# Kernel optimization log

Measured on AMD Instinct MI355X. Metric: run time of the kernel, lower is better.

The kernel has to match this reference:

```python
import jax, jax.numpy as jnp
import numpy as np
import math

TWO_PI = 2.0 * math.pi
B, K, DIM = 8, 1024, 4096
TEMP = 10.0  # softmax temperature from `sims * 10`


def setup_inputs() -> dict:
    key = jax.random.key(0)
    k1, k2 = jax.random.split(key)
    superposed = jax.random.uniform(k1, (B, DIM), jnp.float32, 0.0, TWO_PI)
    codebook = jax.random.uniform(k2, (K, DIM), jnp.float32, 0.0, TWO_PI)
    return {"superposed": superposed, "codebook": codebook, "num_iterations": 50}


def _cos_sim(est, codebook):
    # est: (B, dim), codebook: (K, dim) -> (B, K) mean cosine of phase diff
    return jnp.cos(est[:, None, :] - codebook[None, :, :]).mean(axis=-1)


def reference(superposed, codebook, num_iterations):
    # Batched resonator decode: iteratively refine estimate toward codebook
    # entries via softmax-weighted phasor superposition (torch.angle == atan2).
    cb_cos = jnp.cos(codebook)  # (K, dim) real part of codebook phasors
    cb_sin = jnp.sin(codebook)  # (K, dim) imag part

    def step(est, _):
        sims = _cos_sim(est, codebook)                 # (B, K)
        w = jax.nn.softmax(sims * TEMP, axis=-1)       # (B, K)
        re = w @ cb_cos                                # (B, dim)
        im = w @ cb_sin                                # (B, dim)
        est_new = jnp.arctan2(im, re) % TWO_PI         # angle of complex sum
        return est_new, None

    est, _ = jax.lax.scan(step, superposed, None, length=num_iterations)
    return _cos_sim(est, codebook)  # (B, K) final similarity scores
```

## Files before the change

### kernel.cpp

```cpp
#include <hip/hip_runtime.h>
#include <hip/hip_fp16.h>
#include <math.h>


#define KCODES 1024
#define DIMS   4096
#define BATCH  8
#define NITER_MAX 50
#define NSLICE 256

#define T1_SZF   (DIMS * 2 * KCODES / 2)
#define EST_OFF  (T1_SZF)
#define EST_SZ   (DIMS * 2 * BATCH)
#define W_OFF    (EST_OFF + EST_SZ)
#define W_SZ     (BATCH * KCODES)
#define P_OFF    (W_OFF + W_SZ)

#define C2 (0.00244140625f * 1.4426950408889634f)

__device__ __forceinline__ ushort f2bf(float x) {
  unsigned u = __float_as_uint(x);
  return (ushort)((u + 0x7FFFu + ((u >> 16) & 1u)) >> 16);
}
__device__ __forceinline__ float bf2f(ushort u) {
  return __uint_as_float(((unsigned)u) << 16);
}

template <int CTRL>
__device__ __forceinline__ float dpp_add(float x) {
  int v = __builtin_amdgcn_update_dpp(0, __float_as_int(x), CTRL, 0xF, 0xF, false);
  return x + __int_as_float(v);
}
__device__ __forceinline__ float wave_sum64(float x) {
  x = dpp_add<0x111>(x);
  x = dpp_add<0x112>(x);
  x = dpp_add<0x114>(x);
  x = dpp_add<0x118>(x);
  x = dpp_add<0x142>(x);
  x = dpp_add<0x143>(x);
  return x;
}

__global__ __launch_bounds__(256) void k_trig(const float* __restrict__ cb,
                                              float* __restrict__ ws) {
  __shared__ float lc[64][65], ls[64][65];
  const int t  = threadIdx.x;
  const int bk = blockIdx.x & 15;
  const int bd = blockIdx.x >> 4;
  const int k0 = bk * 64, d0 = bd * 64;
  const int c = t & 63;
  #pragma unroll
  for (int i = 0; i < 16; ++i) {
    const int r = (t >> 6) + i * 4;
    float a = cb[(size_t)(k0 + r) * DIMS + d0 + c];
    float s, cc; sincosf(a, &s, &cc);
    lc[r][c] = cc; ls[r][c] = s;
  }
  __syncthreads();
  ushort* T1 = (ushort*)ws;
  #pragma unroll
  for (int j = 0; j < 16; ++j) {
    const int dd = (t >> 6) + j * 4;
    T1[(size_t)((d0 + dd) * 2 + 0) * KCODES + k0 + c] = f2bf(lc[c][dd]);
    T1[(size_t)((d0 + dd) * 2 + 1) * KCODES + k0 + c] = f2bf(ls[c][dd]);
  }
}

__global__ __launch_bounds__(256) void k_init(const float* __restrict__ sup,
                                              float* __restrict__ ws) {
  float* EST = ws + EST_OFF;
  const int i = blockIdx.x * 256 + threadIdx.x;
  const int b = i >> 12, d = i & 4095;
  float s, c; sincosf(sup[(size_t)b * DIMS + d], &s, &c);
  EST[(d * 2 + 0) * BATCH + b] = c;
  EST[(d * 2 + 1) * BATCH + b] = s;
}

__global__ __launch_bounds__(256) void k_sims0(float* __restrict__ ws) {
  const ushort* T1  = (const ushort*)ws;
  const float*  EST = ws + EST_OFF;
  __half* P = (__half*)(ws + P_OFF);
  const int t  = threadIdx.x;
  const int ds = blockIdx.x;
  const int r0 = ds * 32;
  const int k4 = t * 4;

  float4 acc[BATCH];
  #pragma unroll
  for (int b = 0; b < BATCH; ++b) acc[b] = make_float4(0.f, 0.f, 0.f, 0.f);

  #pragma unroll 8
  for (int r = 0; r < 32; ++r) {
    const int row = r0 + r;
    const ushort4 tu = *(const ushort4*)&T1[(size_t)row * KCODES + k4];
    const float4 tv = make_float4(bf2f(tu.x), bf2f(tu.y), bf2f(tu.z), bf2f(tu.w));
    const float4 e0 = *(const float4*)&EST[row * BATCH + 0];
    const float4 e1 = *(const float4*)&EST[row * BATCH + 4];
    const float ev[8] = {e0.x, e0.y, e0.z, e0.w, e1.x, e1.y, e1.z, e1.w};
    #pragma unroll
    for (int b = 0; b < BATCH; ++b) {
      acc[b].x = fmaf(ev[b], tv.x, acc[b].x);
      acc[b].y = fmaf(ev[b], tv.y, acc[b].y);
      acc[b].z = fmaf(ev[b], tv.z, acc[b].z);
      acc[b].w = fmaf(ev[b], tv.w, acc[b].w);
    }
  }
  #pragma unroll
  for (int b = 0; b < BATCH; ++b) {
    __half* pp = &P[(size_t)ds * (BATCH * KCODES) + b * KCODES + k4];
    *(__half2*)(pp + 0) = __floats2half2_rn(acc[b].x, acc[b].y);
    *(__half2*)(pp + 2) = __floats2half2_rn(acc[b].z, acc[b].w);
  }
}

__global__ __launch_bounds__(256) void k_wexp(float* __restrict__ ws,
                                              const int* __restrict__ nit_p,
                                              int it) {
  if (it >= *nit_p) return;
  const __half* P = (const __half*)(ws + P_OFF);
  float* W = ws + W_OFF;
  __shared__ float scr[128];
  const int t = threadIdx.x, lane = t & 63, wv = t >> 6;
  const int b2 = blockIdx.x >> 5;
  const int k0 = (blockIdx.x & 31) * 32;

  float4 raw[4];
  const float4* p4 =
      (const float4*)(P + (size_t)t * (BATCH * KCODES) + b2 * KCODES + k0);
  raw[0] = p4[0]; raw[1] = p4[1]; raw[2] = p4[2]; raw[3] = p4[3];
  const __half2* h2 = (const __half2*)raw;
  #pragma unroll
  for (int kk = 0; kk < 16; ++kk) {
    const float2 f2 = __half22float2(h2[kk]);
    const float s0 = wave_sum64(f2.x);
    const float s1 = wave_sum64(f2.y);
    if (lane == 63) {
      scr[wv * 32 + 2 * kk + 0] = s0;
      scr[wv * 32 + 2 * kk + 1] = s1;
    }
  }
  __syncthreads();
  if (t < 32) {
    const float s = scr[t] + scr[32 + t] + scr[64 + t] + scr[96 + t];
    W[b2 * KCODES + k0 + t] = exp2f(s * C2);
  }
}

__global__ __launch_bounds__(512) void k_fused(float* __restrict__ ws,
                                               const int* __restrict__ nit_p,
                                               int it) {
  if (it >= *nit_p) return;
  const ushort* T1 = (const ushort*)ws;
  const float*  Wg = ws + W_OFF;
  __half* P = (__half*)(ws + P_OFF);

  __shared__ float smem[BATCH * KCODES];
  __shared__ float est_l[32 * BATCH];

  const int t = threadIdx.x, lane = t & 63, wv = t >> 6;
  const int r0 = blockIdx.x * 32;

  #pragma unroll
  for (int j = 0; j < 4; ++j) {
    const int idx = (j * 512 + t) * 4;
    *(float4*)&smem[idx] = *(const float4*)&Wg[idx];
  }
  __syncthreads();

  const int rw = wv * 4;
  float acc[4][BATCH];
  #pragma unroll
  for (int r = 0; r < 4; ++r)
    #pragma unroll
    for (int b = 0; b < BATCH; ++b) acc[r][b] = 0.f;

  #pragma unroll
  for (int c = 0; c < 4; ++c) {
    const int kk = c * 256 + lane * 4;
    float4 wr[BATCH];
    #pragma unroll
    for (int b = 0; b < BATCH; ++b)
      wr[b] = *(const float4*)&smem[b * KCODES + kk];
    #pragma unroll
    for (int r = 0; r < 4; ++r) {
      const ushort4 tu = *(const ushort4*)&T1[(size_t)(r0 + rw + r) * KCODES + kk];
      const float4 tv = make_float4(bf2f(tu.x), bf2f(tu.y), bf2f(tu.z), bf2f(tu.w));
      #pragma unroll
      for (int b = 0; b < BATCH; ++b) {
        acc[r][b] = fmaf(wr[b].x, tv.x, acc[r][b]);
        acc[r][b] = fmaf(wr[b].y, tv.y, acc[r][b]);
        acc[r][b] = fmaf(wr[b].z, tv.z, acc[r][b]);
        acc[r][b] = fmaf(wr[b].w, tv.w, acc[r][b]);
      }
    }
  }
  #pragma unroll
  for (int r = 0; r < 4; ++r)
    #pragma unroll
    for (int b = 0; b < BATCH; ++b) {
      const float s = wave_sum64(acc[r][b]);
      if (lane == 63) est_l[(rw + r) * BATCH + b] = s;
    }
  __syncthreads();

  if (t < 128) {
    const int dl = t >> 3, b = t & 7;
    const float re = est_l[(2 * dl + 0) * BATCH + b];
    const float im = est_l[(2 * dl + 1) * BATCH + b];
    const float n2 = fmaf(re, re, im * im);
    float ec, es;
    if (n2 > 0.f) {
      const float inv = rsqrtf(n2);
      ec = re * inv; es = im * inv;
    } else { ec = 1.f; es = 0.f; }
    est_l[(2 * dl + 0) * BATCH + b] = ec;
    est_l[(2 * dl + 1) * BATCH + b] = es;
  }
  __syncthreads();

  const int half = t >> 8, tk = t & 255, k4 = tk * 4;
  const int rb = half * 16;
  float4 a[BATCH];
  #pragma unroll
  for (int b = 0; b < BATCH; ++b) a[b] = make_float4(0.f, 0.f, 0.f, 0.f);

  #pragma unroll
  for (int r = 0; r < 16; ++r) {
    const int lr = rb + r;
    const ushort4 tu = *(const ushort4*)&T1[(size_t)(r0 + lr) * KCODES + k4];
    const float4 tv = make_float4(bf2f(tu.x), bf2f(tu.y), bf2f(tu.z), bf2f(tu.w));
    const float4 e0 = *(const float4*)&est_l[lr * BATCH + 0];
    const float4 e1 = *(const float4*)&est_l[lr * BATCH + 4];
    const float ev[8] = {e0.x, e0.y, e0.z, e0.w, e1.x, e1.y, e1.z, e1.w};
    #pragma unroll
    for (int b = 0; b < BATCH; ++b) {
      a[b].x = fmaf(ev[b], tv.x, a[b].x);
      a[b].y = fmaf(ev[b], tv.y, a[b].y);
      a[b].z = fmaf(ev[b], tv.z, a[b].z);
      a[b].w = fmaf(ev[b], tv.w, a[b].w);
    }
  }
  if (half == 1) {
    #pragma unroll
    for (int b = 0; b < BATCH; ++b)
      *(float4*)&smem[(b * 256 + tk) * 4] = a[b];
  }
  __syncthreads();
  if (half == 0) {
    #pragma unroll
    for (int b = 0; b < BATCH; ++b) {
      const float4 o = *(const float4*)&smem[(b * 256 + tk) * 4];
      __half* pp = &P[(size_t)blockIdx.x * (BATCH * KCODES) + b * KCODES + k4];
      *(__half2*)(pp + 0) = __floats2half2_rn(a[b].x + o.x, a[b].y + o.y);
      *(__half2*)(pp + 2) = __floats2half2_rn(a[b].z + o.z, a[b].w + o.w);
    }
  }
}

__global__ __launch_bounds__(256) void k_out(const float* __restrict__ ws,
                                             float* __restrict__ out) {
  const __half* P = (const __half*)(ws + P_OFF);
  __shared__ float scr[128];
  const int t = threadIdx.x, lane = t & 63, wv = t >> 6;
  const int b2 = blockIdx.x >> 5;
  const int k0 = (blockIdx.x & 31) * 32;

  float4 raw[4];
  const float4* p4 =
      (const float4*)(P + (size_t)t * (BATCH * KCODES) + b2 * KCODES + k0);
  raw[0] = p4[0]; raw[1] = p4[1]; raw[2] = p4[2]; raw[3] = p4[3];
  const __half2* h2 = (const __half2*)raw;
  #pragma unroll
  for (int kk = 0; kk < 16; ++kk) {
    const float2 f2 = __half22float2(h2[kk]);
    const float s0 = wave_sum64(f2.x);
    const float s1 = wave_sum64(f2.y);
    if (lane == 63) {
      scr[wv * 32 + 2 * kk + 0] = s0;
      scr[wv * 32 + 2 * kk + 1] = s1;
    }
  }
  __syncthreads();
  if (t < 32) {
    const float s = scr[t] + scr[32 + t] + scr[64 + t] + scr[96 + t];
    out[b2 * KCODES + k0 + t] = s * (1.0f / (float)DIMS);
  }
}

extern "C" void kernel_launch(void* const* d_in, const int* in_sizes, int n_in,
                              void* d_out, int out_size, void* d_ws, size_t ws_size,
                              hipStream_t stream) {
  const float* sup = (const float*)d_in[0];
  const float* cbk = (const float*)d_in[1];
  const int*   nit = (const int*)d_in[2];
  float* outp = (float*)d_out;
  float* ws   = (float*)d_ws;

  hipLaunchKernelGGL(k_trig,  dim3(1024), dim3(256), 0, stream, cbk, ws);
  hipLaunchKernelGGL(k_init,  dim3(128),  dim3(256), 0, stream, sup, ws);
  hipLaunchKernelGGL(k_sims0, dim3(256),  dim3(256), 0, stream, ws);

  for (int it = 0; it < NITER_MAX; ++it) {
    hipLaunchKernelGGL(k_wexp,  dim3(256), dim3(256), 0, stream, ws, nit, it);
    hipLaunchKernelGGL(k_fused, dim3(256), dim3(512), 0, stream, ws, nit, it);
  }
  hipLaunchKernelGGL(k_out, dim3(256), dim3(256), 0, stream, ws, outp);
}
```

Measured before the change: 729.3 us.

## Compute sims per codeword block from transposed table instead of split-K partials

Adds a second bf16 codebook table laid out codeword-major, so each block computes full similarity dot products for four codewords over all dims. The half-precision partial-sum buffer and the separate reduction kernel are removed. The estimate-update kernel now only normalizes and writes the new estimate, and the sim/exp kernel also produces the final output. This drops the partial-sum round trip through global memory and the fp16 rounding of partials. In exchange it doubles table storage, and every block reads the whole estimate vector.

```diff
diff --git a/kernel.cpp b/kernel.cpp
--- a/kernel.cpp
+++ b/kernel.cpp
@@ -1,20 +1,19 @@
 #include <hip/hip_runtime.h>
-#include <hip/hip_fp16.h>
 #include <math.h>
 
 
 #define KCODES 1024
 #define DIMS   4096
 #define BATCH  8
+#define JROWS  (DIMS * 2)
 #define NITER_MAX 50
-#define NSLICE 256
-
-#define T1_SZF   (DIMS * 2 * KCODES / 2)
-#define EST_OFF  (T1_SZF)
-#define EST_SZ   (DIMS * 2 * BATCH)
-#define W_OFF    (EST_OFF + EST_SZ)
-#define W_SZ     (BATCH * KCODES)
-#define P_OFF    (W_OFF + W_SZ)
+
+#define T1_SZF  (JROWS * KCODES / 2)
+#define T2_OFF  (T1_SZF)
+#define T2_SZF  (T1_SZF)
+#define EST_OFF (T2_OFF + T2_SZF)
+#define EST_SZ  (JROWS * BATCH)
+#define W_OFF   (EST_OFF + EST_SZ)
 
 #define C2 (0.00244140625f * 1.4426950408889634f)
 
@@ -66,95 +65,110 @@
   }
 }
 
+__global__ __launch_bounds__(256) void k_trig2(const float* __restrict__ cb,
+                                               float* __restrict__ ws) {
+  __shared__ float cbl[4][DIMS];
+  const int t = threadIdx.x;
+  const int g = blockIdx.x;
+  #pragma unroll
+  for (int c = 0; c < 4; ++c)
+    #pragma unroll
+    for (int q = 0; q < 4; ++q) {
+      const int off = (q * 256 + t) * 4;
+      *(float4*)&cbl[c][off] = *(const float4*)&cb[(size_t)(4 * g + c) * DIMS + off];
+    }
+  __syncthreads();
+
+  ushort buf[128];
+  #pragma unroll
+  for (int dl = 0; dl < 16; ++dl) {
+    #pragma unroll
+    for (int c = 0; c < 4; ++c) {
+      float s, cc; sincosf(cbl[c][16 * t + dl], &s, &cc);
+      buf[(2 * dl + 0) * 4 + c] = f2bf(cc);
+      buf[(2 * dl + 1) * 4 + c] = f2bf(s);
+    }
+  }
+  uint4* dst = (uint4*)((ushort*)(ws + T2_OFF) + (size_t)g * (JROWS * 4) + t * 128);
+  const uint4* src = (const uint4*)buf;
+  #pragma unroll
+  for (int i = 0; i < 16; ++i) dst[i] = src[i];
+}
+
 __global__ __launch_bounds__(256) void k_init(const float* __restrict__ sup,
                                               float* __restrict__ ws) {
   float* EST = ws + EST_OFF;
   const int i = blockIdx.x * 256 + threadIdx.x;
   const int b = i >> 12, d = i & 4095;
   float s, c; sincosf(sup[(size_t)b * DIMS + d], &s, &c);
-  EST[(d * 2 + 0) * BATCH + b] = c;
-  EST[(d * 2 + 1) * BATCH + b] = s;
-}
-
-__global__ __launch_bounds__(256) void k_sims0(float* __restrict__ ws) {
-  const ushort* T1  = (const ushort*)ws;
+  EST[(2 * d + 0) * BATCH + b] = c;
+  EST[(2 * d + 1) * BATCH + b] = s;
+}
+
+__global__ __launch_bounds__(512) void k_simw(float* __restrict__ ws,
+                                              const int* __restrict__ nit_p,
+                                              float* __restrict__ out,
+                                              int it) {
+  const int NI = *nit_p;
+  if (it > NI) return;
+  const ushort* T2  = (const ushort*)(ws + T2_OFF);
   const float*  EST = ws + EST_OFF;
-  __half* P = (__half*)(ws + P_OFF);
-  const int t  = threadIdx.x;
-  const int ds = blockIdx.x;
-  const int r0 = ds * 32;
-  const int k4 = t * 4;
-
-  float4 acc[BATCH];
-  #pragma unroll
-  for (int b = 0; b < BATCH; ++b) acc[b] = make_float4(0.f, 0.f, 0.f, 0.f);
-
-  #pragma unroll 8
-  for (int r = 0; r < 32; ++r) {
-    const int row = r0 + r;
-    const ushort4 tu = *(const ushort4*)&T1[(size_t)row * KCODES + k4];
-    const float4 tv = make_float4(bf2f(tu.x), bf2f(tu.y), bf2f(tu.z), bf2f(tu.w));
-    const float4 e0 = *(const float4*)&EST[row * BATCH + 0];
-    const float4 e1 = *(const float4*)&EST[row * BATCH + 4];
+  float* W = ws + W_OFF;
+  __shared__ float scr[8 * 32];
+
+  const int t = threadIdx.x, lane = t & 63, wv = t >> 6;
+  const int g = blockIdx.x;
+  const ushort* trow = T2 + (size_t)g * (JROWS * 4);
+
+  float acc[4][BATCH];
+  #pragma unroll
+  for (int c = 0; c < 4; ++c)
+    #pragma unroll
+    for (int b = 0; b < BATCH; ++b) acc[c][b] = 0.f;
+
+  #pragma unroll 4
+  for (int i = 0; i < 16; ++i) {
+    const int j = i * 512 + t;
+    const float4 e0 = *(const float4*)&EST[j * BATCH + 0];
+    const float4 e1 = *(const float4*)&EST[j * BATCH + 4];
     const float ev[8] = {e0.x, e0.y, e0.z, e0.w, e1.x, e1.y, e1.z, e1.w};
+    const ushort4 tu = *(const ushort4*)&trow[j * 4];
+    const float tc[4] = {bf2f(tu.x), bf2f(tu.y), bf2f(tu.z), bf2f(tu.w)};
+    #pragma unroll
+    for (int c = 0; c < 4; ++c)
+      #pragma unroll
+      for (int b = 0; b < BATCH; ++b)
+        acc[c][b] = fmaf(tc[c], ev[b], acc[c][b]);
+  }
+
+  #pragma unroll
+  for (int c = 0; c < 4; ++c)
     #pragma unroll
     for (int b = 0; b < BATCH; ++b) {
-      acc[b].x = fmaf(ev[b], tv.x, acc[b].x);
-      acc[b].y = fmaf(ev[b], tv.y, acc[b].y);
-      acc[b].z = fmaf(ev[b], tv.z, acc[b].z);
-      acc[b].w = fmaf(ev[b], tv.w, acc[b].w);
-    }
-  }
-  #pragma unroll
-  for (int b = 0; b < BATCH; ++b) {
-    __half* pp = &P[(size_t)ds * (BATCH * KCODES) + b * KCODES + k4];
-    *(__half2*)(pp + 0) = __floats2half2_rn(acc[b].x, acc[b].y);
-    *(__half2*)(pp + 2) = __floats2half2_rn(acc[b].z, acc[b].w);
-  }
-}
-
-__global__ __launch_bounds__(256) void k_wexp(float* __restrict__ ws,
-                                              const int* __restrict__ nit_p,
-                                              int it) {
-  if (it >= *nit_p) return;
-  const __half* P = (const __half*)(ws + P_OFF);
-  float* W = ws + W_OFF;
-  __shared__ float scr[128];
-  const int t = threadIdx.x, lane = t & 63, wv = t >> 6;
-  const int b2 = blockIdx.x >> 5;
-  const int k0 = (blockIdx.x & 31) * 32;
-
-  float4 raw[4];
-  const float4* p4 =
-      (const float4*)(P + (size_t)t * (BATCH * KCODES) + b2 * KCODES + k0);
-  raw[0] = p4[0]; raw[1] = p4[1]; raw[2] = p4[2]; raw[3] = p4[3];
-  const __half2* h2 = (const __half2*)raw;
-  #pragma unroll
-  for (int kk = 0; kk < 16; ++kk) {
-    const float2 f2 = __half22float2(h2[kk]);
-    const float s0 = wave_sum64(f2.x);
-    const float s1 = wave_sum64(f2.y);
-    if (lane == 63) {
-      scr[wv * 32 + 2 * kk + 0] = s0;
-      scr[wv * 32 + 2 * kk + 1] = s1;
-    }
-  }
-  __syncthreads();
+      const float s = wave_sum64(acc[c][b]);
+      if (lane == 63) scr[wv * 32 + c * BATCH + b] = s;
+    }
+  __syncthreads();
+
   if (t < 32) {
-    const float s = scr[t] + scr[32 + t] + scr[64 + t] + scr[96 + t];
-    W[b2 * KCODES + k0 + t] = exp2f(s * C2);
-  }
-}
-
-__global__ __launch_bounds__(512) void k_fused(float* __restrict__ ws,
-                                               const int* __restrict__ nit_p,
-                                               int it) {
+    float s = 0.f;
+    #pragma unroll
+    for (int w8 = 0; w8 < 8; ++w8) s += scr[w8 * 32 + t];
+    const int c = t >> 3, b = t & 7;
+    if (it == NI) out[b * KCODES + 4 * g + c] = s * (1.0f / (float)DIMS);
+    else          W[b * KCODES + 4 * g + c] = exp2f(s * C2);
+  }
+}
+
+__global__ __launch_bounds__(512) void k_est(float* __restrict__ ws,
+                                             const int* __restrict__ nit_p,
+                                             int it) {
   if (it >= *nit_p) return;
   const ushort* T1 = (const ushort*)ws;
   const float*  Wg = ws + W_OFF;
-  __half* P = (__half*)(ws + P_OFF);
-
-  __shared__ float smem[BATCH * KCODES];
+  float* EST = ws + EST_OFF;
+
+  __shared__ float Wl[BATCH * KCODES];
   __shared__ float est_l[32 * BATCH];
 
   const int t = threadIdx.x, lane = t & 63, wv = t >> 6;
@@ -163,7 +177,7 @@
   #pragma unroll
   for (int j = 0; j < 4; ++j) {
     const int idx = (j * 512 + t) * 4;
-    *(float4*)&smem[idx] = *(const float4*)&Wg[idx];
+    *(float4*)&Wl[idx] = *(const float4*)&Wg[idx];
   }
   __syncthreads();
 
@@ -180,7 +194,7 @@
     float4 wr[BATCH];
     #pragma unroll
     for (int b = 0; b < BATCH; ++b)
-      wr[b] = *(const float4*)&smem[b * KCODES + kk];
+      wr[b] = *(const float4*)&Wl[b * KCODES + kk];
     #pragma unroll
     for (int r = 0; r < 4; ++r) {
       const ushort4 tu = *(const ushort4*)&T1[(size_t)(r0 + rw + r) * KCODES + kk];
@@ -218,73 +232,7 @@
   }
   __syncthreads();
 
-  const int half = t >> 8, tk = t & 255, k4 = tk * 4;
-  const int rb = half * 16;
-  float4 a[BATCH];
-  #pragma unroll
-  for (int b = 0; b < BATCH; ++b) a[b] = make_float4(0.f, 0.f, 0.f, 0.f);
-
-  #pragma unroll
-  for (int r = 0; r < 16; ++r) {
-    const int lr = rb + r;
-    const ushort4 tu = *(const ushort4*)&T1[(size_t)(r0 + lr) * KCODES + k4];
-    const float4 tv = make_float4(bf2f(tu.x), bf2f(tu.y), bf2f(tu.z), bf2f(tu.w));
-    const float4 e0 = *(const float4*)&est_l[lr * BATCH + 0];
-    const float4 e1 = *(const float4*)&est_l[lr * BATCH + 4];
-    const float ev[8] = {e0.x, e0.y, e0.z, e0.w, e1.x, e1.y, e1.z, e1.w};
-    #pragma unroll
-    for (int b = 0; b < BATCH; ++b) {
-      a[b].x = fmaf(ev[b], tv.x, a[b].x);
-      a[b].y = fmaf(ev[b], tv.y, a[b].y);
-      a[b].z = fmaf(ev[b], tv.z, a[b].z);
-      a[b].w = fmaf(ev[b], tv.w, a[b].w);
-    }
-  }
-  if (half == 1) {
-    #pragma unroll
-    for (int b = 0; b < BATCH; ++b)
-      *(float4*)&smem[(b * 256 + tk) * 4] = a[b];
-  }
-  __syncthreads();
-  if (half == 0) {
-    #pragma unroll
-    for (int b = 0; b < BATCH; ++b) {
-      const float4 o = *(const float4*)&smem[(b * 256 + tk) * 4];
-      __half* pp = &P[(size_t)blockIdx.x * (BATCH * KCODES) + b * KCODES + k4];
-      *(__half2*)(pp + 0) = __floats2half2_rn(a[b].x + o.x, a[b].y + o.y);
-      *(__half2*)(pp + 2) = __floats2half2_rn(a[b].z + o.z, a[b].w + o.w);
-    }
-  }
-}
-
-__global__ __launch_bounds__(256) void k_out(const float* __restrict__ ws,
-                                             float* __restrict__ out) {
-  const __half* P = (const __half*)(ws + P_OFF);
-  __shared__ float scr[128];
-  const int t = threadIdx.x, lane = t & 63, wv = t >> 6;
-  const int b2 = blockIdx.x >> 5;
-  const int k0 = (blockIdx.x & 31) * 32;
-
-  float4 raw[4];
-  const float4* p4 =
-      (const float4*)(P + (size_t)t * (BATCH * KCODES) + b2 * KCODES + k0);
-  raw[0] = p4[0]; raw[1] = p4[1]; raw[2] = p4[2]; raw[3] = p4[3];
-  const __half2* h2 = (const __half2*)raw;
-  #pragma unroll
-  for (int kk = 0; kk < 16; ++kk) {
-    const float2 f2 = __half22float2(h2[kk]);
-    const float s0 = wave_sum64(f2.x);
-    const float s1 = wave_sum64(f2.y);
-    if (lane == 63) {
-      scr[wv * 32 + 2 * kk + 0] = s0;
-      scr[wv * 32 + 2 * kk + 1] = s1;
-    }
-  }
-  __syncthreads();
-  if (t < 32) {
-    const float s = scr[t] + scr[32 + t] + scr[64 + t] + scr[96 + t];
-    out[b2 * KCODES + k0 + t] = s * (1.0f / (float)DIMS);
-  }
+  if (t < 256) EST[r0 * BATCH + t] = est_l[t];
 }
 
 extern "C" void kernel_launch(void* const* d_in, const int* in_sizes, int n_in,
@@ -297,12 +245,12 @@
   float* ws   = (float*)d_ws;
 
   hipLaunchKernelGGL(k_trig,  dim3(1024), dim3(256), 0, stream, cbk, ws);
+  hipLaunchKernelGGL(k_trig2, dim3(256),  dim3(256), 0, stream, cbk, ws);
   hipLaunchKernelGGL(k_init,  dim3(128),  dim3(256), 0, stream, sup, ws);
-  hipLaunchKernelGGL(k_sims0, dim3(256),  dim3(256), 0, stream, ws);
 
   for (int it = 0; it < NITER_MAX; ++it) {
-    hipLaunchKernelGGL(k_wexp,  dim3(256), dim3(256), 0, stream, ws, nit, it);
-    hipLaunchKernelGGL(k_fused, dim3(256), dim3(512), 0, stream, ws, nit, it);
-  }
-  hipLaunchKernelGGL(k_out, dim3(256), dim3(256), 0, stream, ws, outp);
-}
+    hipLaunchKernelGGL(k_simw, dim3(256), dim3(512), 0, stream, ws, nit, outp, it);
+    hipLaunchKernelGGL(k_est,  dim3(256), dim3(512), 0, stream, ws, nit, it);
+  }
+  hipLaunchKernelGGL(k_simw, dim3(256), dim3(512), 0, stream, ws, nit, outp, NITER_MAX);
+}
```

Measured after the change: 765.3 us. 1.05x slower.
